# Kernel tuning notes

Measured on AMD Instinct MI355X. Metric: run time of the kernel, lower is better.

## Reference

```python
import jax, jax.numpy as jnp
import numpy as np

G, N, E, B = 4, 100000, 500000, 512
V, D, H, C = 50000, 300, 128, 20
NUM_HEADS, STEPS = 3, 2


def setup_inputs() -> dict:
    key = jax.random.key(0)
    ks = jax.random.split(key, 12)
    return {
        "node_indices": jax.random.randint(ks[0], (G, N), 0, V),
        "src": jax.random.randint(ks[1], (G, E), 0, N),
        "dst": jax.random.randint(ks[2], (G, E), 0, N),
        "node_graph_ids": jnp.sort(jax.random.randint(ks[3], (G, N), 0, B), axis=-1),
        "edge_weights": jax.random.uniform(ks[4], (G, E), dtype=jnp.float32),
        "emb_table": jax.random.normal(ks[5], (V, D), dtype=jnp.float32) * 0.1,
        "edge_params": jnp.ones((G,), dtype=jnp.float32),
        "W_proj": jax.random.normal(ks[6], (G, D, H), dtype=jnp.float32) / np.sqrt(D),
        "b_proj": jnp.zeros((G, H), dtype=jnp.float32),
        "W_cls": jax.random.normal(ks[7], (G, H, C), dtype=jnp.float32) / np.sqrt(H),
        "b_cls": jnp.zeros((G, C), dtype=jnp.float32),
        "W_fuse": jax.random.normal(ks[8], (NUM_HEADS, C, C, G), dtype=jnp.float32) / np.sqrt(C * G),
        "b_fuse": jnp.zeros((NUM_HEADS, C), dtype=jnp.float32),
    }


def _per_graph_logits(idx, s, d, gid, ew, emb_table, ep, Wp, bp, Wc, bc):
    # embedding lookup + input projection: [N, H]
    h = emb_table[idx] @ Wp + bp
    # graph_learning: relu(scalar * edge_weights)
    w = jax.nn.relu(ep * ew)  # [E]
    # in-degree for DGL mean reduce (0 in-edges -> 0 agg)
    deg = jax.ops.segment_sum(jnp.ones_like(ew), d, num_segments=N)
    inv_deg = jnp.where(deg > 0, 1.0 / deg, 0.0)[:, None]  # [N, 1]
    for _ in range(STEPS):
        msg = h[s] * w[:, None]                                   # gather-multiply [E, H]
        agg = jax.ops.segment_sum(msg, d, num_segments=N) * inv_deg  # scatter-mean [N, H]
        h = h + agg
    # dgl.mean_nodes: per-document mean of node features
    cnt = jax.ops.segment_sum(jnp.ones((N,), h.dtype), gid, num_segments=B)
    doc = jax.ops.segment_sum(h, gid, num_segments=B) / jnp.maximum(cnt, 1.0)[:, None]  # [B, H]
    # classify (dropout = identity in eval)
    return jax.nn.relu(doc) @ Wc + bc  # [B, C]


def reference(node_indices, src, dst, node_graph_ids, edge_weights, emb_table,
              edge_params, W_proj, b_proj, W_cls, b_cls, W_fuse, b_fuse):
    per_graph = jax.vmap(_per_graph_logits,
                         in_axes=(0, 0, 0, 0, 0, None, 0, 0, 0, 0, 0))
    logits = per_graph(node_indices, src, dst, node_graph_ids, edge_weights,
                       emb_table, edge_params, W_proj, b_proj, W_cls, b_cls)  # [G, B, C]
    stacked = jnp.transpose(logits, (1, 2, 0))  # [B, C_in, G] (Conv1d input, kernel=G)
    # Conv1d(out=C, in=C, k=G) per head, valid -> length 1, squeezed
    head_out = jnp.einsum('big,hoig->hbo', stacked, W_fuse) + b_fuse[:, None, :]  # [NH, B, C]
    fused_logits = head_out.mean(axis=0)  # [B, C]
    predictions = jax.nn.softmax(fused_logits, axis=-1)
    return predictions, fused_logits
```

## Files before the change

kernel.cpp:

```cpp
#include <hip/hip_runtime.h>

#define G_  4
#define N_  100000
#define E_  500000
#define B_  512
#define V_  50000
#define D_  300
#define H_  128
#define C_  20
#define NH_ 3

#define KP_  320
#define SCB_  512
#define NBLK_ ((N_ + SCB_ - 1) / SCB_)

#define AROWS_  32
#define APITCH_ 320

typedef unsigned short ushort_t;
typedef __attribute__((ext_vector_type(8))) short bf16x8;
typedef __attribute__((ext_vector_type(4))) float f32x4;

__device__ __forceinline__ ushort_t f2bf(float f) {
    unsigned int x = __float_as_uint(f);
    unsigned int r = x + 0x7FFFu + ((x >> 16) & 1u);
    return (ushort_t)(r >> 16);
}

__device__ __forceinline__ int lower_bound_i(const int* __restrict__ a, int n, int v) {
    int lo = 0, hi = n;
    while (lo < hi) {
        int mid = (lo + hi) >> 1;
        if (a[mid] < v) lo = mid + 1; else hi = mid;
    }
    return lo;
}

__device__ __forceinline__ void unpack8(uint4 u, float* f) {
    f[0] = __uint_as_float((u.x & 0xFFFFu) << 16);
    f[1] = __uint_as_float(u.x & 0xFFFF0000u);
    f[2] = __uint_as_float((u.y & 0xFFFFu) << 16);
    f[3] = __uint_as_float(u.y & 0xFFFF0000u);
    f[4] = __uint_as_float((u.z & 0xFFFFu) << 16);
    f[5] = __uint_as_float(u.z & 0xFFFF0000u);
    f[6] = __uint_as_float((u.w & 0xFFFFu) << 16);
    f[7] = __uint_as_float(u.w & 0xFFFF0000u);
}

__global__ __launch_bounds__(256) void convert_w_kernel(
    const float* __restrict__ Wp,
    ushort_t* __restrict__ Wt)
{
    int flat = blockIdx.x * 256 + threadIdx.x;
    int g = flat / (H_ * KP_);
    int r = flat % (H_ * KP_);
    int n = r / KP_;
    int k = r % KP_;
    float v = (k < D_) ? Wp[((size_t)g * D_ + k) * H_ + n] : 0.f;
    Wt[flat] = f2bf(v);
}

template <int NG>
__global__ __launch_bounds__(256) void mfma_gemm_async_kernel(
    const float* __restrict__ emb,
    const ushort_t* __restrict__ Wt,
    const float* __restrict__ bp,
    ushort_t* __restrict__ Ph)
{
    __shared__ float As[AROWS_ * APITCH_];

    const int t    = threadIdx.x;
    const int w    = t >> 6;
    const int l    = t & 63;
    const int l16  = l & 15;
    const int lk   = (l >> 4) * 8;
    const int ch   = w * 32;
    const int rowbase = blockIdx.x * AROWS_;

#pragma unroll
    for (int j = 0; j < 10; ++j) {
        const int call      = w * 10 + j;
        const int flat_byte = call * 1024 + l * 16;
        const int r         = flat_byte / 1280;
        const int q_sw      = (flat_byte - r * 1280) >> 4;
        int q_un = q_sw ^ (r & 7);
        int koff = q_un << 4;
        if (koff >= 1200) koff = 0;
        int grow = rowbase + r;
        if (grow > V_ - 1) grow = V_ - 1;
        const float* gsrc = emb + (size_t)grow * D_ + (koff >> 2);
        __builtin_amdgcn_global_load_lds(
            (const __attribute__((address_space(1))) void*)gsrc,
            (__attribute__((address_space(3))) void*)(As + call * 256),
            16, 0, 0);
    }
    __syncthreads();

    f32x4 acc[NG][2][2];
#pragma unroll
    for (int g = 0; g < NG; ++g)
#pragma unroll
        for (int m = 0; m < 2; ++m)
#pragma unroll
            for (int n = 0; n < 2; ++n) acc[g][m][n] = (f32x4){0.f, 0.f, 0.f, 0.f};

#pragma unroll
    for (int k0i = 0; k0i < 10; ++k0i) {
        const int k0 = k0i * 32;

        bf16x8 a[2];
#pragma unroll
        for (int m = 0; m < 2; ++m) {
            const int r  = m * 16 + l16;
            const int q0 = (k0 + lk) >> 2;
            const int s  = r & 7;
            float4 x0 = *reinterpret_cast<const float4*>(
                &As[r * APITCH_ + ((q0 ^ s) << 2)]);
            float4 x1 = *reinterpret_cast<const float4*>(
                &As[r * APITCH_ + (((q0 + 1) ^ s) << 2)]);
            a[m][0] = (short)f2bf(x0.x); a[m][1] = (short)f2bf(x0.y);
            a[m][2] = (short)f2bf(x0.z); a[m][3] = (short)f2bf(x0.w);
            a[m][4] = (short)f2bf(x1.x); a[m][5] = (short)f2bf(x1.y);
            a[m][6] = (short)f2bf(x1.z); a[m][7] = (short)f2bf(x1.w);
        }

        const int kb = k0 + lk;
#pragma unroll
        for (int g = 0; g < NG; ++g) {
            const ushort_t* Wg = Wt + (size_t)g * H_ * KP_;
            bf16x8 b[2];
#pragma unroll
            for (int n = 0; n < 2; ++n)
                b[n] = *reinterpret_cast<const bf16x8*>(
                    &Wg[(size_t)(ch + n * 16 + l16) * KP_ + kb]);
#pragma unroll
            for (int m = 0; m < 2; ++m)
#pragma unroll
                for (int n = 0; n < 2; ++n)
                    acc[g][m][n] = __builtin_amdgcn_mfma_f32_16x16x32_bf16(
                        a[m], b[n], acc[g][m][n], 0, 0, 0);
        }
    }

    const int rbase = (l >> 4) * 4;
#pragma unroll
    for (int g = 0; g < NG; ++g) {
        ushort_t* Pg = Ph + (size_t)g * V_ * H_;
#pragma unroll
        for (int n = 0; n < 2; ++n) {
            const int col  = ch + n * 16 + l16;
            const float bv = bp[g * H_ + col];
#pragma unroll
            for (int m = 0; m < 2; ++m) {
#pragma unroll
                for (int r = 0; r < 4; ++r) {
                    int row = rowbase + m * 16 + rbase + r;
                    if (row < V_)
                        Pg[(size_t)row * H_ + col] = f2bf(acc[g][m][n][r] + bv);
                }
            }
        }
    }
}

__global__ __launch_bounds__(256) void deg_count_kernel(const int* __restrict__ dstA,
                                                        int* __restrict__ deg)
{
    const int g = blockIdx.y;
    int e = blockIdx.x * 256 + threadIdx.x;
    if (e < E_) atomicAdd(&deg[g * N_ + dstA[(size_t)g * E_ + e]], 1);
}

__global__ __launch_bounds__(512) void scan1_kernel(const int* __restrict__ deg,
                                                    int* __restrict__ bsum)
{
    __shared__ int sh[512];
    const int g = blockIdx.y, b = blockIdx.x, t = threadIdx.x;
    int i = b * SCB_ + t;
    sh[t] = (i < N_) ? deg[g * N_ + i] : 0;
    __syncthreads();
#pragma unroll
    for (int ofs = 256; ofs > 0; ofs >>= 1) {
        if (t < ofs) sh[t] += sh[t + ofs];
        __syncthreads();
    }
    if (t == 0) bsum[g * NBLK_ + b] = sh[0];
}

__global__ __launch_bounds__(256) void scan2_kernel(const int* __restrict__ bsum,
                                                    int* __restrict__ bpre,
                                                    int* __restrict__ off)
{
    __shared__ int sh[256];
    const int g = blockIdx.x, t = threadIdx.x;
    int v = (t < NBLK_) ? bsum[g * NBLK_ + t] : 0;
    sh[t] = v;
    __syncthreads();
#pragma unroll
    for (int ofs = 1; ofs < 256; ofs <<= 1) {
        int u = (t >= ofs) ? sh[t - ofs] : 0;
        __syncthreads();
        sh[t] += u;
        __syncthreads();
    }
    if (t < NBLK_) bpre[g * (NBLK_ + 1) + t + 1] = sh[t];
    if (t == 0) {
        bpre[g * (NBLK_ + 1)] = 0;
        off[(size_t)g * (N_ + 1) + N_] = sh[NBLK_ - 1];
    }
}

__global__ __launch_bounds__(512) void scan3_kernel(int* __restrict__ deg,
                                                    const int* __restrict__ bpre,
                                                    int* __restrict__ off)
{
    __shared__ int sh[512];
    const int g = blockIdx.y, b = blockIdx.x, t = threadIdx.x;
    int i = b * SCB_ + t;
    int v = (i < N_) ? deg[g * N_ + i] : 0;
    sh[t] = v;
    __syncthreads();
#pragma unroll
    for (int ofs = 1; ofs < 512; ofs <<= 1) {
        int u = (t >= ofs) ? sh[t - ofs] : 0;
        __syncthreads();
        sh[t] += u;
        __syncthreads();
    }
    if (i < N_) {
        off[(size_t)g * (N_ + 1) + i] = bpre[g * (NBLK_ + 1) + b] + sh[t] - v;
        deg[g * N_ + i] = 0;
    }
}

__global__ __launch_bounds__(256) void scatter_kernel(
    const int* __restrict__ srcA, const int* __restrict__ dstA,
    const float* __restrict__ ewA, const float* __restrict__ ep,
    const int* __restrict__ idxA, const int* __restrict__ off,
    int* __restrict__ cnt, int4* __restrict__ csr4)
{
    const int g = blockIdx.y;
    int e = blockIdx.x * 256 + threadIdx.x;
    if (e >= E_) return;
    int s = srcA[(size_t)g * E_ + e];
    int d = dstA[(size_t)g * E_ + e];
    int pos = off[(size_t)g * (N_ + 1) + d] + atomicAdd(&cnt[g * N_ + d], 1);
    float w = ep[g] * ewA[(size_t)g * E_ + e];
    csr4[(size_t)g * E_ + pos] =
        make_int4(s, idxA[(size_t)g * N_ + s], __float_as_int(fmaxf(w, 0.f)), 0);
}

__global__ __launch_bounds__(256) void prop1_kernel(
    const int* __restrict__ idx_g, const int* __restrict__ off,
    const int4* __restrict__ csr4,
    const ushort_t* __restrict__ Ph, ushort_t* __restrict__ hBh)
{
    const int n = blockIdx.x * 16 + (threadIdx.x >> 4);
    if (n >= N_) return;
    const int lane = threadIdx.x & 15;
    const int col  = lane * 8;

    const int lo = off[n], hi = off[n + 1];

    float sf[8];
    unpack8(*reinterpret_cast<const uint4*>(&Ph[(size_t)idx_g[n] * H_ + col]), sf);

    float acc[8];
#pragma unroll
    for (int j = 0; j < 8; ++j) acc[j] = 0.f;

    int i = lo;
    for (; i + 4 <= hi; i += 4) {
        int4 e0 = csr4[i],     e1 = csr4[i + 1];
        int4 e2 = csr4[i + 2], e3 = csr4[i + 3];
        float c0 = __int_as_float(e0.z), c1 = __int_as_float(e1.z);
        float c2 = __int_as_float(e2.z), c3 = __int_as_float(e3.z);
        uint4 u0 = *reinterpret_cast<const uint4*>(&Ph[(size_t)e0.y * H_ + col]);
        uint4 u1 = *reinterpret_cast<const uint4*>(&Ph[(size_t)e1.y * H_ + col]);
        uint4 u2 = *reinterpret_cast<const uint4*>(&Ph[(size_t)e2.y * H_ + col]);
        uint4 u3 = *reinterpret_cast<const uint4*>(&Ph[(size_t)e3.y * H_ + col]);
        float f0[8], f1[8], f2[8], f3[8];
        unpack8(u0, f0); unpack8(u1, f1); unpack8(u2, f2); unpack8(u3, f3);
#pragma unroll
        for (int j = 0; j < 8; ++j)
            acc[j] += c0 * f0[j] + c1 * f1[j] + c2 * f2[j] + c3 * f3[j];
    }
    for (; i < hi; ++i) {
        int4 e0 = csr4[i];
        float c = __int_as_float(e0.z);
        float f[8];
        unpack8(*reinterpret_cast<const uint4*>(&Ph[(size_t)e0.y * H_ + col]), f);
#pragma unroll
        for (int j = 0; j < 8; ++j) acc[j] += c * f[j];
    }

    const float inv = (hi > lo) ? 1.0f / (float)(hi - lo) : 0.f;
    ushort_t p[8];
#pragma unroll
    for (int j = 0; j < 8; ++j) p[j] = f2bf(sf[j] + inv * acc[j]);
    uint4 o;
    o.x = (unsigned)p[0] | ((unsigned)p[1] << 16);
    o.y = (unsigned)p[2] | ((unsigned)p[3] << 16);
    o.z = (unsigned)p[4] | ((unsigned)p[5] << 16);
    o.w = (unsigned)p[6] | ((unsigned)p[7] << 16);
    *reinterpret_cast<uint4*>(&hBh[(size_t)n * H_ + col]) = o;
}

__global__ __launch_bounds__(256) void prop2_fused_kernel(
    const int* __restrict__ off, const int4* __restrict__ csr4,
    const int* __restrict__ gid,
    const ushort_t* __restrict__ hBh, float* __restrict__ docsum)
{
    const int nloc = threadIdx.x >> 4;
    const int n    = blockIdx.x * 16 + nloc;
    const int lane = threadIdx.x & 15;
    const int col  = lane * 8;

    __shared__ float sh[16][H_];
    __shared__ int   shgid[16];

    float o[8];
    if (n < N_) {
        const int lo = off[n], hi = off[n + 1];

        float sf[8];
        unpack8(*reinterpret_cast<const uint4*>(&hBh[(size_t)n * H_ + col]), sf);

        float acc[8];
#pragma unroll
        for (int j = 0; j < 8; ++j) acc[j] = 0.f;

        int i = lo;
        for (; i + 4 <= hi; i += 4) {
            int4 e0 = csr4[i],     e1 = csr4[i + 1];
            int4 e2 = csr4[i + 2], e3 = csr4[i + 3];
            float c0 = __int_as_float(e0.z), c1 = __int_as_float(e1.z);
            float c2 = __int_as_float(e2.z), c3 = __int_as_float(e3.z);
            uint4 u0 = *reinterpret_cast<const uint4*>(&hBh[(size_t)e0.x * H_ + col]);
            uint4 u1 = *reinterpret_cast<const uint4*>(&hBh[(size_t)e1.x * H_ + col]);
            uint4 u2 = *reinterpret_cast<const uint4*>(&hBh[(size_t)e2.x * H_ + col]);
            uint4 u3 = *reinterpret_cast<const uint4*>(&hBh[(size_t)e3.x * H_ + col]);
            float f0[8], f1[8], f2[8], f3[8];
            unpack8(u0, f0); unpack8(u1, f1); unpack8(u2, f2); unpack8(u3, f3);
#pragma unroll
            for (int j = 0; j < 8; ++j)
                acc[j] += c0 * f0[j] + c1 * f1[j] + c2 * f2[j] + c3 * f3[j];
        }
        for (; i < hi; ++i) {
            int4 e0 = csr4[i];
            float c = __int_as_float(e0.z);
            float f[8];
            unpack8(*reinterpret_cast<const uint4*>(&hBh[(size_t)e0.x * H_ + col]), f);
#pragma unroll
            for (int j = 0; j < 8; ++j) acc[j] += c * f[j];
        }

        const float inv = (hi > lo) ? 1.0f / (float)(hi - lo) : 0.f;
#pragma unroll
        for (int j = 0; j < 8; ++j) o[j] = sf[j] + inv * acc[j];
        if (lane == 0) shgid[nloc] = gid[n];
    } else {
#pragma unroll
        for (int j = 0; j < 8; ++j) o[j] = 0.f;
        if (lane == 0) shgid[nloc] = -1;
    }

#pragma unroll
    for (int j = 0; j < 8; ++j) sh[nloc][col + j] = o[j];
    __syncthreads();

    const int c  = threadIdx.x & 127;
    const int q  = threadIdx.x >> 7;
    const int n0 = q * 8;
    float run = 0.f;
    int rgid = shgid[n0];
    for (int k = 0; k < 8; ++k) {
        int gk = shgid[n0 + k];
        if (gk != rgid) {
            if (rgid >= 0) atomicAdd(&docsum[(size_t)rgid * H_ + c], run);
            run = 0.f; rgid = gk;
        }
        run += sh[n0 + k][c];
    }
    if (rgid >= 0) atomicAdd(&docsum[(size_t)rgid * H_ + c], run);
}

__global__ __launch_bounds__(128) void cls_kernel(
    const int* __restrict__ gidA, const float* __restrict__ docsum,
    const float* __restrict__ Wc, const float* __restrict__ bc,
    float* __restrict__ logits)
{
    const int b   = blockIdx.x;
    const int g   = blockIdx.y;
    const int tid = threadIdx.x;
    const int* gid = gidA + (size_t)g * N_;

    int lo = lower_bound_i(gid, N_, b);
    int hi = lower_bound_i(gid, N_, b + 1);
    float cnt = (float)(hi - lo);

    __shared__ float sdoc[H_];
    float dv = docsum[((size_t)g * B_ + b) * H_ + tid] / fmaxf(cnt, 1.0f);
    sdoc[tid] = fmaxf(dv, 0.f);
    __syncthreads();

    if (tid < C_) {
        const float* Wcg = Wc + (size_t)g * H_ * C_;
        float acc = bc[g * C_ + tid];
#pragma unroll 8
        for (int hh = 0; hh < H_; ++hh) acc += sdoc[hh] * Wcg[hh * C_ + tid];
        logits[((size_t)g * B_ + b) * C_ + tid] = acc;
    }
}

__global__ __launch_bounds__(64) void fuse_kernel(
    const float* __restrict__ logits,
    const float* __restrict__ Wf,
    const float* __restrict__ bf,
    float* __restrict__ out)
{
    const int b   = blockIdx.x;
    const int tid = threadIdx.x;

    __shared__ float s[C_ * G_];
    __shared__ float fl[C_];

    for (int t = tid; t < C_ * G_; t += 64) {
        int i = t >> 2, g = t & 3;
        s[t] = logits[((long)g * B_ + b) * C_ + i];
    }
    __syncthreads();

    if (tid < C_) {
        float acc = 0.f;
        for (int hd = 0; hd < NH_; ++hd) {
            float a = bf[hd * C_ + tid];
            const float* wrow = &Wf[((hd * C_ + tid) * C_) * G_];
#pragma unroll 5
            for (int i = 0; i < C_; ++i) {
#pragma unroll
                for (int g = 0; g < G_; ++g)
                    a += s[i * G_ + g] * wrow[i * G_ + g];
            }
            acc += a;
        }
        fl[tid] = acc * (1.0f / 3.0f);
    }
    __syncthreads();

    if (tid < C_) {
        float f = fl[tid];
        float m = -1e30f;
#pragma unroll
        for (int i = 0; i < C_; ++i) m = fmaxf(m, fl[i]);
        float ssum = 0.f;
#pragma unroll
        for (int i = 0; i < C_; ++i) ssum += expf(fl[i] - m);
        out[b * C_ + tid] = expf(f - m) / ssum;
        out[B_ * C_ + b * C_ + tid] = f;
    }
}

extern "C" void kernel_launch(void* const* d_in, const int* in_sizes, int n_in,
                              void* d_out, int out_size, void* d_ws, size_t ws_size,
                              hipStream_t stream)
{
    const int*   node_indices = (const int*)d_in[0];
    const int*   srcA         = (const int*)d_in[1];
    const int*   dstA         = (const int*)d_in[2];
    const int*   gidA         = (const int*)d_in[3];
    const float* ewA          = (const float*)d_in[4];
    const float* emb          = (const float*)d_in[5];
    const float* ep           = (const float*)d_in[6];
    const float* Wp           = (const float*)d_in[7];
    const float* bp           = (const float*)d_in[8];
    const float* Wc           = (const float*)d_in[9];
    const float* bc           = (const float*)d_in[10];
    const float* Wf           = (const float*)d_in[11];
    const float* bf           = (const float*)d_in[12];
    float*       out          = (float*)d_out;

    char* wp0 = (char*)d_ws;
    auto alloc = [&](size_t bytes) {
        void* r = (void*)wp0;
        wp0 += (bytes + 255) & ~(size_t)255;
        return r;
    };
    ushort_t* hBh      = (ushort_t*)alloc((size_t)N_ * H_ * 2);
    float*    docsum   = (float*)   alloc((size_t)G_ * B_ * H_ * 4);
    float*    logits   = (float*)   alloc((size_t)G_ * B_ * C_ * 4);
    ushort_t* Wt       = (ushort_t*)alloc((size_t)G_ * H_ * KP_ * 2);
    int*      deg_i    = (int*)     alloc((size_t)G_ * N_ * 4);
    int*      off      = (int*)     alloc((size_t)G_ * (N_ + 1) * 4);
    int*      bsum     = (int*)     alloc((size_t)G_ * NBLK_ * 4);
    int*      bpre     = (int*)     alloc((size_t)G_ * (NBLK_ + 1) * 4);
    int4*     csr4     = (int4*)    alloc((size_t)G_ * E_ * 16);

    const size_t pbytes = (size_t)V_ * H_ * 2;
    size_t used  = (size_t)(wp0 - (char*)d_ws);
    size_t avail = (ws_size > used) ? ws_size - used : 0;

    int ng;
    if (avail >= 4 * pbytes + 1024)      ng = 4;
    else if (avail >= 2 * pbytes + 1024) ng = 2;
    else                                 ng = 1;
    ushort_t* Ph = (ushort_t*)alloc((size_t)ng * pbytes);

    convert_w_kernel<<<(G_ * H_ * KP_) / 256, 256, 0, stream>>>(Wp, Wt);
    hipMemsetAsync(docsum, 0, (size_t)G_ * B_ * H_ * sizeof(float), stream);

    hipMemsetAsync(deg_i, 0, (size_t)G_ * N_ * sizeof(int), stream);
    deg_count_kernel<<<dim3((E_ + 255) / 256, G_), 256, 0, stream>>>(dstA, deg_i);
    scan1_kernel<<<dim3(NBLK_, G_), 512, 0, stream>>>(deg_i, bsum);
    scan2_kernel<<<G_, 256, 0, stream>>>(bsum, bpre, off);
    scan3_kernel<<<dim3(NBLK_, G_), 512, 0, stream>>>(deg_i, bpre, off);
    scatter_kernel<<<dim3((E_ + 255) / 256, G_), 256, 0, stream>>>(
        srcA, dstA, ewA, ep, node_indices, off, deg_i, csr4);

    const int gemm_blocks = (V_ + AROWS_ - 1) / AROWS_;
    for (int gbase = 0; gbase < G_; gbase += ng) {
        const ushort_t* Wtg = Wt + (size_t)gbase * H_ * KP_;
        const float*    bpg = bp + (size_t)gbase * H_;
        if (ng == 4)
            mfma_gemm_async_kernel<4><<<gemm_blocks, 256, 0, stream>>>(emb, Wtg, bpg, Ph);
        else if (ng == 2)
            mfma_gemm_async_kernel<2><<<gemm_blocks, 256, 0, stream>>>(emb, Wtg, bpg, Ph);
        else
            mfma_gemm_async_kernel<1><<<gemm_blocks, 256, 0, stream>>>(emb, Wtg, bpg, Ph);

        for (int gi = 0; gi < ng; ++gi) {
            const int g = gbase + gi;
            const int*      idx   = node_indices + (size_t)g * N_;
            const int*      gid   = gidA + (size_t)g * N_;
            const int*      off_g = off + (size_t)g * (N_ + 1);
            const int4*     csr_g = csr4 + (size_t)g * E_;
            const ushort_t* Pg    = Ph + (size_t)gi * V_ * H_;

            prop1_kernel<<<(N_ + 15) / 16, 256, 0, stream>>>(
                idx, off_g, csr_g, Pg, hBh);
            prop2_fused_kernel<<<(N_ + 15) / 16, 256, 0, stream>>>(
                off_g, csr_g, gid, hBh, docsum + (size_t)g * B_ * H_);
        }
    }

    cls_kernel<<<dim3(B_, G_), 128, 0, stream>>>(gidA, docsum, Wc, bc, logits);
    fuse_kernel<<<B_, 64, 0, stream>>>(logits, Wf, bf, out);
}
```

Before: 530.5 us.

## Fuse embedding GEMM and CSR scatter into one interleaved launch

Merges the memory-bound CSR scatter kernel and the MFMA projection GEMM into one horizontally fused launch. Every sixth block runs a GEMM tile and the rest run scatter work, so compute-heavy and atomic/latency-heavy blocks share the GPU at once. The scatter's CSR writes also switch to nontemporal stores. The fused kernel reserves the GEMM's shared memory for every block, which can limit occupancy for the scatter blocks, and it is only used when the workspace fits all four projections.

```diff
diff --git a/kernel.cpp b/kernel.cpp
--- a/kernel.cpp
+++ b/kernel.cpp
@@ -17,9 +17,14 @@
 #define AROWS_  32
 #define APITCH_ 320
 
+#define GEMM_BLKS_ ((V_ + AROWS_ - 1) / AROWS_)
+#define SBLK_      ((E_ + 255) / 256)
+#define FUSE_TOT_  (GEMM_BLKS_ + SBLK_ * G_)
+
 typedef unsigned short ushort_t;
 typedef __attribute__((ext_vector_type(8))) short bf16x8;
 typedef __attribute__((ext_vector_type(4))) float f32x4;
+typedef __attribute__((ext_vector_type(4))) int   i32x4;
 
 __device__ __forceinline__ ushort_t f2bf(float f) {
     unsigned int x = __float_as_uint(f);
@@ -61,21 +66,18 @@
 }
 
 template <int NG>
-__global__ __launch_bounds__(256) void mfma_gemm_async_kernel(
-    const float* __restrict__ emb,
-    const ushort_t* __restrict__ Wt,
-    const float* __restrict__ bp,
-    ushort_t* __restrict__ Ph)
-{
-    __shared__ float As[AROWS_ * APITCH_];
-
+__device__ __forceinline__ void gemm_body(
+    float* As, int bx,
+    const float* __restrict__ emb, const ushort_t* __restrict__ Wt,
+    const float* __restrict__ bp, ushort_t* __restrict__ Ph)
+{
     const int t    = threadIdx.x;
     const int w    = t >> 6;
     const int l    = t & 63;
     const int l16  = l & 15;
     const int lk   = (l >> 4) * 8;
     const int ch   = w * 32;
-    const int rowbase = blockIdx.x * AROWS_;
+    const int rowbase = bx * AROWS_;
 
 #pragma unroll
     for (int j = 0; j < 10; ++j) {
@@ -163,6 +165,64 @@
     }
 }
 
+__device__ __forceinline__ void scatter_body(
+    int g, int e,
+    const int* __restrict__ srcA, const int* __restrict__ dstA,
+    const float* __restrict__ ewA, const float* __restrict__ ep,
+    const int* __restrict__ idxA, const int* __restrict__ off,
+    int* __restrict__ cnt, i32x4* __restrict__ csr4)
+{
+    if (e >= E_) return;
+    int s = srcA[(size_t)g * E_ + e];
+    int d = dstA[(size_t)g * E_ + e];
+    int pos = off[(size_t)g * (N_ + 1) + d] + atomicAdd(&cnt[g * N_ + d], 1);
+    float w = ep[g] * ewA[(size_t)g * E_ + e];
+    i32x4 v = { s, idxA[(size_t)g * N_ + s],
+                __float_as_int(fmaxf(w, 0.f)), 0 };
+    __builtin_nontemporal_store(v, &csr4[(size_t)g * E_ + pos]);
+}
+
+__global__ __launch_bounds__(256) void gemm_scatter_fused_kernel(
+    const float* __restrict__ emb, const ushort_t* __restrict__ Wt,
+    const float* __restrict__ bp, ushort_t* __restrict__ Ph,
+    const int* __restrict__ srcA, const int* __restrict__ dstA,
+    const float* __restrict__ ewA, const float* __restrict__ ep,
+    const int* __restrict__ idxA, const int* __restrict__ off,
+    int* __restrict__ cnt, i32x4* __restrict__ csr4)
+{
+    __shared__ float As[AROWS_ * APITCH_];
+
+    const int b = blockIdx.x;
+    if ((b % 6 == 0) && (b / 6 < GEMM_BLKS_)) {
+        gemm_body<4>(As, b / 6, emb, Wt, bp, Ph);
+    } else {
+        const int nGemmBefore = min((b + 5) / 6, GEMM_BLKS_);
+        const int s = b - nGemmBefore;
+        const int g = s / SBLK_;
+        const int e = (s % SBLK_) * 256 + threadIdx.x;
+        scatter_body(g, e, srcA, dstA, ewA, ep, idxA, off, cnt, csr4);
+    }
+}
+
+template <int NG>
+__global__ __launch_bounds__(256) void mfma_gemm_async_kernel(
+    const float* __restrict__ emb, const ushort_t* __restrict__ Wt,
+    const float* __restrict__ bp, ushort_t* __restrict__ Ph)
+{
+    __shared__ float As[AROWS_ * APITCH_];
+    gemm_body<NG>(As, blockIdx.x, emb, Wt, bp, Ph);
+}
+
+__global__ __launch_bounds__(256) void scatter_kernel(
+    const int* __restrict__ srcA, const int* __restrict__ dstA,
+    const float* __restrict__ ewA, const float* __restrict__ ep,
+    const int* __restrict__ idxA, const int* __restrict__ off,
+    int* __restrict__ cnt, i32x4* __restrict__ csr4)
+{
+    scatter_body(blockIdx.y, blockIdx.x * 256 + threadIdx.x,
+                 srcA, dstA, ewA, ep, idxA, off, cnt, csr4);
+}
+
 __global__ __launch_bounds__(256) void deg_count_kernel(const int* __restrict__ dstA,
                                                         int* __restrict__ deg)
 {
@@ -231,23 +291,6 @@
         off[(size_t)g * (N_ + 1) + i] = bpre[g * (NBLK_ + 1) + b] + sh[t] - v;
         deg[g * N_ + i] = 0;
     }
-}
-
-__global__ __launch_bounds__(256) void scatter_kernel(
-    const int* __restrict__ srcA, const int* __restrict__ dstA,
-    const float* __restrict__ ewA, const float* __restrict__ ep,
-    const int* __restrict__ idxA, const int* __restrict__ off,
-    int* __restrict__ cnt, int4* __restrict__ csr4)
-{
-    const int g = blockIdx.y;
-    int e = blockIdx.x * 256 + threadIdx.x;
-    if (e >= E_) return;
-    int s = srcA[(size_t)g * E_ + e];
-    int d = dstA[(size_t)g * E_ + e];
-    int pos = off[(size_t)g * (N_ + 1) + d] + atomicAdd(&cnt[g * N_ + d], 1);
-    float w = ep[g] * ewA[(size_t)g * E_ + e];
-    csr4[(size_t)g * E_ + pos] =
-        make_int4(s, idxA[(size_t)g * N_ + s], __float_as_int(fmaxf(w, 0.f)), 0);
 }
 
 __global__ __launch_bounds__(256) void prop1_kernel(
@@ -494,7 +537,7 @@
     int*      off      = (int*)     alloc((size_t)G_ * (N_ + 1) * 4);
     int*      bsum     = (int*)     alloc((size_t)G_ * NBLK_ * 4);
     int*      bpre     = (int*)     alloc((size_t)G_ * (NBLK_ + 1) * 4);
-    int4*     csr4     = (int4*)    alloc((size_t)G_ * E_ * 16);
+    i32x4*    csr4     = (i32x4*)   alloc((size_t)G_ * E_ * 16);
 
     const size_t pbytes = (size_t)V_ * H_ * 2;
     size_t used  = (size_t)(wp0 - (char*)d_ws);
@@ -514,33 +557,50 @@
     scan1_kernel<<<dim3(NBLK_, G_), 512, 0, stream>>>(deg_i, bsum);
     scan2_kernel<<<G_, 256, 0, stream>>>(bsum, bpre, off);
     scan3_kernel<<<dim3(NBLK_, G_), 512, 0, stream>>>(deg_i, bpre, off);
-    scatter_kernel<<<dim3((E_ + 255) / 256, G_), 256, 0, stream>>>(
-        srcA, dstA, ewA, ep, node_indices, off, deg_i, csr4);
-
-    const int gemm_blocks = (V_ + AROWS_ - 1) / AROWS_;
-    for (int gbase = 0; gbase < G_; gbase += ng) {
-        const ushort_t* Wtg = Wt + (size_t)gbase * H_ * KP_;
-        const float*    bpg = bp + (size_t)gbase * H_;
-        if (ng == 4)
-            mfma_gemm_async_kernel<4><<<gemm_blocks, 256, 0, stream>>>(emb, Wtg, bpg, Ph);
-        else if (ng == 2)
-            mfma_gemm_async_kernel<2><<<gemm_blocks, 256, 0, stream>>>(emb, Wtg, bpg, Ph);
-        else
-            mfma_gemm_async_kernel<1><<<gemm_blocks, 256, 0, stream>>>(emb, Wtg, bpg, Ph);
-
-        for (int gi = 0; gi < ng; ++gi) {
-            const int g = gbase + gi;
+
+    if (ng == 4) {
+        gemm_scatter_fused_kernel<<<FUSE_TOT_, 256, 0, stream>>>(
+            emb, Wt, bp, Ph, srcA, dstA, ewA, ep, node_indices, off,
+            deg_i, csr4);
+
+        for (int g = 0; g < G_; ++g) {
             const int*      idx   = node_indices + (size_t)g * N_;
             const int*      gid   = gidA + (size_t)g * N_;
             const int*      off_g = off + (size_t)g * (N_ + 1);
-            const int4*     csr_g = csr4 + (size_t)g * E_;
-            const ushort_t* Pg    = Ph + (size_t)gi * V_ * H_;
+            const int4*     csr_g = (const int4*)csr4 + (size_t)g * E_;
+            const ushort_t* Pg    = Ph + (size_t)g * V_ * H_;
 
             prop1_kernel<<<(N_ + 15) / 16, 256, 0, stream>>>(
                 idx, off_g, csr_g, Pg, hBh);
             prop2_fused_kernel<<<(N_ + 15) / 16, 256, 0, stream>>>(
                 off_g, csr_g, gid, hBh, docsum + (size_t)g * B_ * H_);
         }
+    } else {
+        scatter_kernel<<<dim3(SBLK_, G_), 256, 0, stream>>>(
+            srcA, dstA, ewA, ep, node_indices, off, deg_i, csr4);
+
+        for (int gbase = 0; gbase < G_; gbase += ng) {
+            const ushort_t* Wtg = Wt + (size_t)gbase * H_ * KP_;
+            const float*    bpg = bp + (size_t)gbase * H_;
+            if (ng == 2)
+                mfma_gemm_async_kernel<2><<<GEMM_BLKS_, 256, 0, stream>>>(emb, Wtg, bpg, Ph);
+            else
+                mfma_gemm_async_kernel<1><<<GEMM_BLKS_, 256, 0, stream>>>(emb, Wtg, bpg, Ph);
+
+            for (int gi = 0; gi < ng; ++gi) {
+                const int g = gbase + gi;
+                const int*      idx   = node_indices + (size_t)g * N_;
+                const int*      gid   = gidA + (size_t)g * N_;
+                const int*      off_g = off + (size_t)g * (N_ + 1);
+                const int4*     csr_g = (const int4*)csr4 + (size_t)g * E_;
+                const ushort_t* Pg    = Ph + (size_t)gi * V_ * H_;
+
+                prop1_kernel<<<(N_ + 15) / 16, 256, 0, stream>>>(
+                    idx, off_g, csr_g, Pg, hBh);
+                prop2_fused_kernel<<<(N_ + 15) / 16, 256, 0, stream>>>(
+                    off_g, csr_g, gid, hBh, docsum + (size_t)g * B_ * H_);
+            }
+        }
     }
 
     cls_kernel<<<dim3(B_, G_), 128, 0, stream>>>(gidA, docsum, Wc, bc, logits);
```

New measurement: 544.2 us. 1.03x slower.
